# Kernel optimization log

Measured on AMD Instinct MI355X. Metric: run time of the kernel, lower is better.

Reference implementation:

```python
import jax, jax.numpy as jnp
import numpy as np

NUM_CLASSES = 80
NUM_TOP_QUERIES = 300


def setup_inputs() -> dict:
    key = jax.random.key(0)
    k1, k2, k3 = jax.random.split(key, 3)
    N, Q, K = 256, 1000, NUM_CLASSES
    logits = jax.random.normal(k1, (N, Q, K), dtype=jnp.float32)
    boxes = jax.random.uniform(k2, (N, Q, 4), dtype=jnp.float32)  # cxcywh in [0,1]
    original_sizes = jax.random.randint(k3, (N, 2), 1, 1280, dtype=jnp.int32)  # (h, w)
    return {"logits": logits, "boxes": boxes, "original_sizes": original_sizes}


def reference(logits, boxes, original_sizes):
    # cxcywh -> xywh (top-left x,y plus w,h)
    cxcy, wh = boxes[..., :2], boxes[..., 2:]
    boxes_xy = jnp.concatenate([cxcy - wh * 0.5, wh], axis=-1)  # (N, Q, 4)
    # torch code uses only original_sizes[0], flipped (h,w)->(w,h), tiled to (w,h,w,h)
    sizes_wh = jnp.tile(original_sizes[0][::-1].astype(boxes.dtype), 2)  # (4,)
    boxes_xy = boxes_xy * sizes_wh
    # sigmoid scores, flatten class dim into query dim, top-k over Q*K
    N = logits.shape[0]
    scores_flat = jax.nn.sigmoid(logits).reshape(N, -1)  # (N, Q*K)
    scores, index = jax.lax.top_k(scores_flat, NUM_TOP_QUERIES)  # (N, 300)
    labels = index % NUM_CLASSES
    qidx = index // NUM_CLASSES
    # gather selected boxes per batch row
    sel_boxes = jax.vmap(lambda b, i: b[i])(boxes_xy, qidx)  # (N, 300, 4)
    out = jnp.concatenate(
        [labels[..., None].astype(scores.dtype), scores[..., None], sel_boxes], axis=-1
    )  # (N, 300, 6): (class_id, confidence, x, y, w, h)
    return out
```

## Files before the change

kernel.cpp:

```cpp
#include <hip/hip_runtime.h>
#include <stdint.h>


#define TOPK 300
#define NCLS 80
#define NQ 1000
#define QK (NQ * NCLS)
#define NB 2048
#define CAP 2048
#define THREADS 1024
#define LAST_VALID 544
#define T0F 2.4f
#define RNB 512
#define RSH 14

typedef unsigned long long u64;

__device__ __forceinline__ uint32_t ordf(float f) {
  uint32_t u = __float_as_uint(f);
  return (u & 0x80000000u) ? ~u : (u | 0x80000000u);
}
__device__ __forceinline__ float unordf(uint32_t o) {
  uint32_t u = (o & 0x80000000u) ? (o & 0x7fffffffu) : ~o;
  return __uint_as_float(u);
}

__device__ __forceinline__ void rank_emit(
    const u64 key, const uint32_t bin, const uint32_t* rcur,
    const uint32_t* rh, const u64* buf2, const float* boxes, float* out,
    const int n, const float s0, const float s1) {
  const uint32_t end = rcur[bin];
  const uint32_t beg = end - rh[bin];
  uint32_t rank = beg;
  for (uint32_t q = beg; q < end; ++q) rank += (uint32_t)(buf2[q] > key);
  if (rank < TOPK) {
    const uint32_t u = (uint32_t)(key >> 32);
    const uint32_t idx = ~(uint32_t)(key & 0xffffffffu);
    const float lgv = unordf(u);
    const float score = 1.0f / (1.0f + expf(-lgv));
    const uint32_t q = idx / NCLS;
    const uint32_t lab = idx - q * NCLS;
    const float4 b4 = *(const float4*)(boxes + ((size_t)n * NQ + q) * 4);
    float* op = out + ((size_t)n * TOPK + rank) * 6;
    float2* op2 = (float2*)op;
    op2[0] = make_float2((float)lab, score);
    op2[1] = make_float2((b4.x - 0.5f * b4.z) * s1, (b4.y - 0.5f * b4.w) * s0);
    op2[2] = make_float2(b4.z * s1, b4.w * s0);
  }
}

__global__ __launch_bounds__(THREADS) void detr_post_kernel(
    const float* __restrict__ logits, const float* __restrict__ boxes,
    const int* __restrict__ osz, float* __restrict__ out) {
  __shared__ u64 buf[CAP];
  __shared__ u64 smem64[4096];
  __shared__ uint32_t histf[NB];
  __shared__ uint32_t sh_sel[3];
  __shared__ uint32_t sh_cnt;

  uint32_t* const hist4 = (uint32_t*)smem64;
  u64* const buf2 = smem64;
  uint32_t* const rh = (uint32_t*)(smem64 + 2048);
  uint32_t* const rcur = (uint32_t*)(smem64 + 2304);

  const int n = blockIdx.x;
  const int t = threadIdx.x;
  const float* lg = logits + (size_t)n * QK;

  if (t == 0) sh_cnt = 0;
  if (t < RNB) rh[t] = 0;
  __syncthreads();

#pragma unroll 5
  for (int j = 0; j < 19; ++j) {
    const int i = 4 * t + 4096 * j;
    const float4 v = *(const float4*)(lg + i);
    if (v.x >= T0F) {
      const uint32_t p = atomicAdd(&sh_cnt, 1u);
      if (p < CAP) buf[p] = ((u64)ordf(v.x) << 32) | (u64)(~(uint32_t)(i + 0));
    }
    if (v.y >= T0F) {
      const uint32_t p = atomicAdd(&sh_cnt, 1u);
      if (p < CAP) buf[p] = ((u64)ordf(v.y) << 32) | (u64)(~(uint32_t)(i + 1));
    }
    if (v.z >= T0F) {
      const uint32_t p = atomicAdd(&sh_cnt, 1u);
      if (p < CAP) buf[p] = ((u64)ordf(v.z) << 32) | (u64)(~(uint32_t)(i + 2));
    }
    if (v.w >= T0F) {
      const uint32_t p = atomicAdd(&sh_cnt, 1u);
      if (p < CAP) buf[p] = ((u64)ordf(v.w) << 32) | (u64)(~(uint32_t)(i + 3));
    }
  }
  if (t < LAST_VALID) {
    const int i = 4 * t + 4096 * 19;
    const float4 v = *(const float4*)(lg + i);
    if (v.x >= T0F) {
      const uint32_t p = atomicAdd(&sh_cnt, 1u);
      if (p < CAP) buf[p] = ((u64)ordf(v.x) << 32) | (u64)(~(uint32_t)(i + 0));
    }
    if (v.y >= T0F) {
      const uint32_t p = atomicAdd(&sh_cnt, 1u);
      if (p < CAP) buf[p] = ((u64)ordf(v.y) << 32) | (u64)(~(uint32_t)(i + 1));
    }
    if (v.z >= T0F) {
      const uint32_t p = atomicAdd(&sh_cnt, 1u);
      if (p < CAP) buf[p] = ((u64)ordf(v.z) << 32) | (u64)(~(uint32_t)(i + 2));
    }
    if (v.w >= T0F) {
      const uint32_t p = atomicAdd(&sh_cnt, 1u);
      if (p < CAP) buf[p] = ((u64)ordf(v.w) << 32) | (u64)(~(uint32_t)(i + 3));
    }
  }
  __syncthreads();

  uint32_t cnt = sh_cnt;
  const bool fast_ok = (cnt >= TOPK && cnt <= CAP);
  uint32_t baseord = ordf(T0F);

  if (!fast_ok) {
    uint32_t T = 0, S_above = 0, Krem = TOPK;
    int prev_shift = 32;
    const uint32_t sub = (uint32_t)(t & 3);
    const int shifts[3] = {21, 10, 0};
    const int nbns[3] = {2048, 2048, 1024};

    for (int lvl = 0; lvl < 3; ++lvl) {
      const int sh = shifts[lvl];
      const uint32_t nb = (uint32_t)nbns[lvl];

      for (int b = t; b < NB * 4; b += THREADS) hist4[b] = 0;
      __syncthreads();
      for (int j = 0; j < 20; ++j) {
        if (j == 19 && t >= LAST_VALID) break;
        const int i = 4 * t + 4096 * j;
        const float4 v = *(const float4*)(lg + i);
        const float vs[4] = {v.x, v.y, v.z, v.w};
        for (int c = 0; c < 4; ++c) {
          const uint32_t u = ordf(vs[c]);
          if (lvl == 0 || (u >> prev_shift) == (T >> prev_shift))
            atomicAdd(&hist4[(((u >> sh) & (nb - 1)) << 2) | sub], 1u);
        }
      }
      __syncthreads();

      for (uint32_t b = t; b < nb; b += (uint32_t)THREADS) {
        const uint32_t i4 = b << 2;
        histf[b] = hist4[i4] + hist4[i4 + 1] + hist4[i4 + 2] + hist4[i4 + 3];
      }
      __syncthreads();

      for (uint32_t off = 1; off < nb; off <<= 1) {
        uint32_t a0 = histf[t] + ((t + off < nb) ? histf[t + off] : 0u);
        uint32_t a1 = 0;
        if (nb > (uint32_t)THREADS) {
          const uint32_t i1 = (uint32_t)t + THREADS;
          a1 = histf[i1] + ((i1 + off < nb) ? histf[i1 + off] : 0u);
        }
        __syncthreads();
        histf[t] = a0;
        if (nb > (uint32_t)THREADS) histf[(uint32_t)t + THREADS] = a1;
        __syncthreads();
      }

      for (uint32_t b = t; b < nb; b += (uint32_t)THREADS) {
        const uint32_t s = histf[b];
        const uint32_t sn = (b + 1 < nb) ? histf[b + 1] : 0u;
        if (s >= Krem && sn < Krem) {
          sh_sel[0] = b;
          sh_sel[1] = sn;
          sh_sel[2] = s;
        }
      }
      __syncthreads();
      const uint32_t bsel = sh_sel[0], above = sh_sel[1], candL = sh_sel[2];
      __syncthreads();

      T |= bsel << sh;
      if (S_above + candL <= CAP || lvl == 2) break;
      S_above += above;
      Krem -= above;
      prev_shift = sh;
    }

    if (t == 0) sh_cnt = 0;
    __syncthreads();
    if (t < RNB) rh[t] = 0;
    for (int j = 0; j < 20; ++j) {
      if (j == 19 && t >= LAST_VALID) break;
      const int i = 4 * t + 4096 * j;
      const float4 v = *(const float4*)(lg + i);
      const float vs[4] = {v.x, v.y, v.z, v.w};
      for (int c = 0; c < 4; ++c) {
        const uint32_t u = ordf(vs[c]);
        if (u >= T) {
          const uint32_t p = atomicAdd(&sh_cnt, 1u);
          if (p < CAP) buf[p] = ((u64)u << 32) | (u64)(~(uint32_t)(i + c));
        }
      }
    }
    __syncthreads();
    cnt = sh_cnt < CAP ? sh_cnt : CAP;
    baseord = T;
  }

  const u64 k0 = ((uint32_t)t < cnt) ? buf[t] : 0ULL;
  const u64 k1 = ((uint32_t)(t + THREADS) < cnt) ? buf[t + THREADS] : 0ULL;
  uint32_t b0 = 0, b1 = 0;
  if ((uint32_t)t < cnt) {
    b0 = ((uint32_t)(k0 >> 32) - baseord) >> RSH;
    if (b0 > RNB - 1u) b0 = RNB - 1u;
    atomicAdd(&rh[b0], 1u);
  }
  if ((uint32_t)(t + THREADS) < cnt) {
    b1 = ((uint32_t)(k1 >> 32) - baseord) >> RSH;
    if (b1 > RNB - 1u) b1 = RNB - 1u;
    atomicAdd(&rh[b1], 1u);
  }
  __syncthreads();

  if (t < 64) {
    const uint4 a = *(const uint4*)&rh[8 * t];
    const uint4 b = *(const uint4*)&rh[8 * t + 4];
    const uint32_t c0 = a.x, c1 = a.y, c2 = a.z, c3 = a.w;
    const uint32_t c4 = b.x, c5 = b.y, c6 = b.z, c7 = b.w;
    const uint32_t mysum = c0 + c1 + c2 + c3 + c4 + c5 + c6 + c7;
    uint32_t s = mysum;
    for (int d = 1; d < 64; d <<= 1) {
      const uint32_t o = __shfl_down(s, d);
      if (t + d < 64) s += o;
    }
    uint32_t acc = s - mysum;
    rcur[8 * t + 7] = acc; acc += c7;
    rcur[8 * t + 6] = acc; acc += c6;
    rcur[8 * t + 5] = acc; acc += c5;
    rcur[8 * t + 4] = acc; acc += c4;
    rcur[8 * t + 3] = acc; acc += c3;
    rcur[8 * t + 2] = acc; acc += c2;
    rcur[8 * t + 1] = acc; acc += c1;
    rcur[8 * t + 0] = acc;
  }
  __syncthreads();

  if ((uint32_t)t < cnt) {
    const uint32_t s = atomicAdd(&rcur[b0], 1u);
    buf2[s] = k0;
  }
  if ((uint32_t)(t + THREADS) < cnt) {
    const uint32_t s = atomicAdd(&rcur[b1], 1u);
    buf2[s] = k1;
  }
  __syncthreads();

  const float s0 = (float)osz[0];
  const float s1 = (float)osz[1];

  if ((uint32_t)t < cnt)
    rank_emit(k0, b0, rcur, rh, buf2, boxes, out, n, s0, s1);
  if ((uint32_t)(t + THREADS) < cnt)
    rank_emit(k1, b1, rcur, rh, buf2, boxes, out, n, s0, s1);
}

extern "C" void kernel_launch(void* const* d_in, const int* in_sizes, int n_in,
                              void* d_out, int out_size, void* d_ws, size_t ws_size,
                              hipStream_t stream) {
  const float* logits = (const float*)d_in[0];
  const float* boxes = (const float*)d_in[1];
  const int* osz = (const int*)d_in[2];
  float* out = (float*)d_out;
  const int nbatch = in_sizes[0] / QK;
  detr_post_kernel<<<nbatch, THREADS, 0, stream>>>(logits, boxes, osz, out);
}
```

Before: 124.4 us.

## Split threshold scan into multi-block kernel writing candidates to workspace

```diff
diff --git a/kernel.cpp b/kernel.cpp
--- a/kernel.cpp
+++ b/kernel.cpp
@@ -14,6 +14,11 @@
 #define RNB 512
 #define RSH 14
 
+#define SBLK 8
+#define STHREADS 256
+#define SCHUNK 10000
+#define SLAST 196
+
 typedef unsigned long long u64;
 
 __device__ __forceinline__ uint32_t ordf(float f) {
@@ -23,6 +28,51 @@
 __device__ __forceinline__ float unordf(uint32_t o) {
   uint32_t u = (o & 0x80000000u) ? (o & 0x7fffffffu) : ~o;
   return __uint_as_float(u);
+}
+__device__ __forceinline__ u64 mkkey(uint32_t ord, uint32_t idx) {
+  return ((u64)ord << 32) | (u64)(~idx);
+}
+
+__global__ __launch_bounds__(STHREADS) void zero_kernel(
+    uint32_t* __restrict__ cnts, int nbatch) {
+  const int i = blockIdx.x * STHREADS + threadIdx.x;
+  if (i < nbatch) cnts[i] = 0;
+}
+
+__global__ __launch_bounds__(STHREADS) void scan_kernel(
+    const float* __restrict__ logits, u64* __restrict__ cand,
+    uint32_t* __restrict__ cnts) {
+  const int n = blockIdx.x >> 3;
+  const int rb = blockIdx.x & 7;
+  const int t = threadIdx.x;
+  const int coff = rb * SCHUNK;
+  const float* lg = logits + (size_t)n * QK + coff;
+  u64* cnd = cand + (size_t)n * CAP;
+  uint32_t* cp = cnts + n;
+
+#pragma unroll
+  for (int j = 0; j < 10; ++j) {
+    if (j == 9 && t >= SLAST) break;
+    const int i = 4 * (t + STHREADS * j);
+    const float4 v = *(const float4*)(lg + i);
+    const int gi = coff + i;
+    if (v.x >= T0F) {
+      const uint32_t p = atomicAdd(cp, 1u);
+      if (p < CAP) cnd[p] = mkkey(ordf(v.x), (uint32_t)(gi + 0));
+    }
+    if (v.y >= T0F) {
+      const uint32_t p = atomicAdd(cp, 1u);
+      if (p < CAP) cnd[p] = mkkey(ordf(v.y), (uint32_t)(gi + 1));
+    }
+    if (v.z >= T0F) {
+      const uint32_t p = atomicAdd(cp, 1u);
+      if (p < CAP) cnd[p] = mkkey(ordf(v.z), (uint32_t)(gi + 2));
+    }
+    if (v.w >= T0F) {
+      const uint32_t p = atomicAdd(cp, 1u);
+      if (p < CAP) cnd[p] = mkkey(ordf(v.w), (uint32_t)(gi + 3));
+    }
+  }
 }
 
 __device__ __forceinline__ void rank_emit(
@@ -49,9 +99,10 @@
   }
 }
 
-__global__ __launch_bounds__(THREADS) void detr_post_kernel(
+__global__ __launch_bounds__(THREADS) void rank_kernel(
     const float* __restrict__ logits, const float* __restrict__ boxes,
-    const int* __restrict__ osz, float* __restrict__ out) {
+    const int* __restrict__ osz, float* __restrict__ out,
+    const u64* __restrict__ cand, const uint32_t* __restrict__ cnts) {
   __shared__ u64 buf[CAP];
   __shared__ u64 smem64[4096];
   __shared__ uint32_t histf[NB];
@@ -67,58 +118,20 @@
   const int t = threadIdx.x;
   const float* lg = logits + (size_t)n * QK;
 
-  if (t == 0) sh_cnt = 0;
   if (t < RNB) rh[t] = 0;
-  __syncthreads();
-
-#pragma unroll 5
-  for (int j = 0; j < 19; ++j) {
-    const int i = 4 * t + 4096 * j;
-    const float4 v = *(const float4*)(lg + i);
-    if (v.x >= T0F) {
-      const uint32_t p = atomicAdd(&sh_cnt, 1u);
-      if (p < CAP) buf[p] = ((u64)ordf(v.x) << 32) | (u64)(~(uint32_t)(i + 0));
-    }
-    if (v.y >= T0F) {
-      const uint32_t p = atomicAdd(&sh_cnt, 1u);
-      if (p < CAP) buf[p] = ((u64)ordf(v.y) << 32) | (u64)(~(uint32_t)(i + 1));
-    }
-    if (v.z >= T0F) {
-      const uint32_t p = atomicAdd(&sh_cnt, 1u);
-      if (p < CAP) buf[p] = ((u64)ordf(v.z) << 32) | (u64)(~(uint32_t)(i + 2));
-    }
-    if (v.w >= T0F) {
-      const uint32_t p = atomicAdd(&sh_cnt, 1u);
-      if (p < CAP) buf[p] = ((u64)ordf(v.w) << 32) | (u64)(~(uint32_t)(i + 3));
-    }
-  }
-  if (t < LAST_VALID) {
-    const int i = 4 * t + 4096 * 19;
-    const float4 v = *(const float4*)(lg + i);
-    if (v.x >= T0F) {
-      const uint32_t p = atomicAdd(&sh_cnt, 1u);
-      if (p < CAP) buf[p] = ((u64)ordf(v.x) << 32) | (u64)(~(uint32_t)(i + 0));
-    }
-    if (v.y >= T0F) {
-      const uint32_t p = atomicAdd(&sh_cnt, 1u);
-      if (p < CAP) buf[p] = ((u64)ordf(v.y) << 32) | (u64)(~(uint32_t)(i + 1));
-    }
-    if (v.z >= T0F) {
-      const uint32_t p = atomicAdd(&sh_cnt, 1u);
-      if (p < CAP) buf[p] = ((u64)ordf(v.z) << 32) | (u64)(~(uint32_t)(i + 2));
-    }
-    if (v.w >= T0F) {
-      const uint32_t p = atomicAdd(&sh_cnt, 1u);
-      if (p < CAP) buf[p] = ((u64)ordf(v.w) << 32) | (u64)(~(uint32_t)(i + 3));
-    }
-  }
-  __syncthreads();
-
-  uint32_t cnt = sh_cnt;
+
+  uint32_t cnt = cnts[n];
   const bool fast_ok = (cnt >= TOPK && cnt <= CAP);
   uint32_t baseord = ordf(T0F);
 
-  if (!fast_ok) {
+  u64 k0 = 0, k1 = 0;
+  if (fast_ok) {
+    const u64* cnd = cand + (size_t)n * CAP;
+    if ((uint32_t)t < cnt) k0 = cnd[t];
+    if ((uint32_t)(t + THREADS) < cnt) k1 = cnd[t + THREADS];
+    __syncthreads();
+  } else {
+    __syncthreads();
     uint32_t T = 0, S_above = 0, Krem = TOPK;
     int prev_shift = 32;
     const uint32_t sub = (uint32_t)(t & 3);
@@ -195,17 +208,17 @@
         const uint32_t u = ordf(vs[c]);
         if (u >= T) {
           const uint32_t p = atomicAdd(&sh_cnt, 1u);
-          if (p < CAP) buf[p] = ((u64)u << 32) | (u64)(~(uint32_t)(i + c));
+          if (p < CAP) buf[p] = mkkey(u, (uint32_t)(i + c));
         }
       }
     }
     __syncthreads();
     cnt = sh_cnt < CAP ? sh_cnt : CAP;
     baseord = T;
-  }
-
-  const u64 k0 = ((uint32_t)t < cnt) ? buf[t] : 0ULL;
-  const u64 k1 = ((uint32_t)(t + THREADS) < cnt) ? buf[t + THREADS] : 0ULL;
+    if ((uint32_t)t < cnt) k0 = buf[t];
+    if ((uint32_t)(t + THREADS) < cnt) k1 = buf[t + THREADS];
+  }
+
   uint32_t b0 = 0, b1 = 0;
   if ((uint32_t)t < cnt) {
     b0 = ((uint32_t)(k0 >> 32) - baseord) >> RSH;
@@ -261,6 +274,218 @@
     rank_emit(k1, b1, rcur, rh, buf2, boxes, out, n, s0, s1);
 }
 
+__global__ __launch_bounds__(THREADS) void detr_post_mono(
+    const float* __restrict__ logits, const float* __restrict__ boxes,
+    const int* __restrict__ osz, float* __restrict__ out) {
+  __shared__ u64 buf[CAP];
+  __shared__ u64 smem64[4096];
+  __shared__ uint32_t histf[NB];
+  __shared__ uint32_t sh_sel[3];
+  __shared__ uint32_t sh_cnt;
+
+  uint32_t* const hist4 = (uint32_t*)smem64;
+  u64* const buf2 = smem64;
+  uint32_t* const rh = (uint32_t*)(smem64 + 2048);
+  uint32_t* const rcur = (uint32_t*)(smem64 + 2304);
+
+  const int n = blockIdx.x;
+  const int t = threadIdx.x;
+  const float* lg = logits + (size_t)n * QK;
+
+  if (t == 0) sh_cnt = 0;
+  if (t < RNB) rh[t] = 0;
+  __syncthreads();
+
+#pragma unroll 5
+  for (int j = 0; j < 19; ++j) {
+    const int i = 4 * t + 4096 * j;
+    const float4 v = *(const float4*)(lg + i);
+    if (v.x >= T0F) {
+      const uint32_t p = atomicAdd(&sh_cnt, 1u);
+      if (p < CAP) buf[p] = mkkey(ordf(v.x), (uint32_t)(i + 0));
+    }
+    if (v.y >= T0F) {
+      const uint32_t p = atomicAdd(&sh_cnt, 1u);
+      if (p < CAP) buf[p] = mkkey(ordf(v.y), (uint32_t)(i + 1));
+    }
+    if (v.z >= T0F) {
+      const uint32_t p = atomicAdd(&sh_cnt, 1u);
+      if (p < CAP) buf[p] = mkkey(ordf(v.z), (uint32_t)(i + 2));
+    }
+    if (v.w >= T0F) {
+      const uint32_t p = atomicAdd(&sh_cnt, 1u);
+      if (p < CAP) buf[p] = mkkey(ordf(v.w), (uint32_t)(i + 3));
+    }
+  }
+  if (t < LAST_VALID) {
+    const int i = 4 * t + 4096 * 19;
+    const float4 v = *(const float4*)(lg + i);
+    if (v.x >= T0F) {
+      const uint32_t p = atomicAdd(&sh_cnt, 1u);
+      if (p < CAP) buf[p] = mkkey(ordf(v.x), (uint32_t)(i + 0));
+    }
+    if (v.y >= T0F) {
+      const uint32_t p = atomicAdd(&sh_cnt, 1u);
+      if (p < CAP) buf[p] = mkkey(ordf(v.y), (uint32_t)(i + 1));
+    }
+    if (v.z >= T0F) {
+      const uint32_t p = atomicAdd(&sh_cnt, 1u);
+      if (p < CAP) buf[p] = mkkey(ordf(v.z), (uint32_t)(i + 2));
+    }
+    if (v.w >= T0F) {
+      const uint32_t p = atomicAdd(&sh_cnt, 1u);
+      if (p < CAP) buf[p] = mkkey(ordf(v.w), (uint32_t)(i + 3));
+    }
+  }
+  __syncthreads();
+
+  uint32_t cnt = sh_cnt;
+  const bool fast_ok = (cnt >= TOPK && cnt <= CAP);
+  uint32_t baseord = ordf(T0F);
+
+  if (!fast_ok) {
+    uint32_t T = 0, S_above = 0, Krem = TOPK;
+    int prev_shift = 32;
+    const uint32_t sub = (uint32_t)(t & 3);
+    const int shifts[3] = {21, 10, 0};
+    const int nbns[3] = {2048, 2048, 1024};
+
+    for (int lvl = 0; lvl < 3; ++lvl) {
+      const int sh = shifts[lvl];
+      const uint32_t nb = (uint32_t)nbns[lvl];
+
+      for (int b = t; b < NB * 4; b += THREADS) hist4[b] = 0;
+      __syncthreads();
+      for (int j = 0; j < 20; ++j) {
+        if (j == 19 && t >= LAST_VALID) break;
+        const int i = 4 * t + 4096 * j;
+        const float4 v = *(const float4*)(lg + i);
+        const float vs[4] = {v.x, v.y, v.z, v.w};
+        for (int c = 0; c < 4; ++c) {
+          const uint32_t u = ordf(vs[c]);
+          if (lvl == 0 || (u >> prev_shift) == (T >> prev_shift))
+            atomicAdd(&hist4[(((u >> sh) & (nb - 1)) << 2) | sub], 1u);
+        }
+      }
+      __syncthreads();
+
+      for (uint32_t b = t; b < nb; b += (uint32_t)THREADS) {
+        const uint32_t i4 = b << 2;
+        histf[b] = hist4[i4] + hist4[i4 + 1] + hist4[i4 + 2] + hist4[i4 + 3];
+      }
+      __syncthreads();
+
+      for (uint32_t off = 1; off < nb; off <<= 1) {
+        uint32_t a0 = histf[t] + ((t + off < nb) ? histf[t + off] : 0u);
+        uint32_t a1 = 0;
+        if (nb > (uint32_t)THREADS) {
+          const uint32_t i1 = (uint32_t)t + THREADS;
+          a1 = histf[i1] + ((i1 + off < nb) ? histf[i1 + off] : 0u);
+        }
+        __syncthreads();
+        histf[t] = a0;
+        if (nb > (uint32_t)THREADS) histf[(uint32_t)t + THREADS] = a1;
+        __syncthreads();
+      }
+
+      for (uint32_t b = t; b < nb; b += (uint32_t)THREADS) {
+        const uint32_t s = histf[b];
+        const uint32_t sn = (b + 1 < nb) ? histf[b + 1] : 0u;
+        if (s >= Krem && sn < Krem) {
+          sh_sel[0] = b;
+          sh_sel[1] = sn;
+          sh_sel[2] = s;
+        }
+      }
+      __syncthreads();
+      const uint32_t bsel = sh_sel[0], above = sh_sel[1], candL = sh_sel[2];
+      __syncthreads();
+
+      T |= bsel << sh;
+      if (S_above + candL <= CAP || lvl == 2) break;
+      S_above += above;
+      Krem -= above;
+      prev_shift = sh;
+    }
+
+    if (t == 0) sh_cnt = 0;
+    __syncthreads();
+    if (t < RNB) rh[t] = 0;
+    for (int j = 0; j < 20; ++j) {
+      if (j == 19 && t >= LAST_VALID) break;
+      const int i = 4 * t + 4096 * j;
+      const float4 v = *(const float4*)(lg + i);
+      const float vs[4] = {v.x, v.y, v.z, v.w};
+      for (int c = 0; c < 4; ++c) {
+        const uint32_t u = ordf(vs[c]);
+        if (u >= T) {
+          const uint32_t p = atomicAdd(&sh_cnt, 1u);
+          if (p < CAP) buf[p] = mkkey(u, (uint32_t)(i + c));
+        }
+      }
+    }
+    __syncthreads();
+    cnt = sh_cnt < CAP ? sh_cnt : CAP;
+    baseord = T;
+  }
+
+  const u64 k0 = ((uint32_t)t < cnt) ? buf[t] : 0ULL;
+  const u64 k1 = ((uint32_t)(t + THREADS) < cnt) ? buf[t + THREADS] : 0ULL;
+  uint32_t b0 = 0, b1 = 0;
+  if ((uint32_t)t < cnt) {
+    b0 = ((uint32_t)(k0 >> 32) - baseord) >> RSH;
+    if (b0 > RNB - 1u) b0 = RNB - 1u;
+    atomicAdd(&rh[b0], 1u);
+  }
+  if ((uint32_t)(t + THREADS) < cnt) {
+    b1 = ((uint32_t)(k1 >> 32) - baseord) >> RSH;
+    if (b1 > RNB - 1u) b1 = RNB - 1u;
+    atomicAdd(&rh[b1], 1u);
+  }
+  __syncthreads();
+
+  if (t < 64) {
+    const uint4 a = *(const uint4*)&rh[8 * t];
+    const uint4 b = *(const uint4*)&rh[8 * t + 4];
+    const uint32_t c0 = a.x, c1 = a.y, c2 = a.z, c3 = a.w;
+    const uint32_t c4 = b.x, c5 = b.y, c6 = b.z, c7 = b.w;
+    const uint32_t mysum = c0 + c1 + c2 + c3 + c4 + c5 + c6 + c7;
+    uint32_t s = mysum;
+    for (int d = 1; d < 64; d <<= 1) {
+      const uint32_t o = __shfl_down(s, d);
+      if (t + d < 64) s += o;
+    }
+    uint32_t acc = s - mysum;
+    rcur[8 * t + 7] = acc; acc += c7;
+    rcur[8 * t + 6] = acc; acc += c6;
+    rcur[8 * t + 5] = acc; acc += c5;
+    rcur[8 * t + 4] = acc; acc += c4;
+    rcur[8 * t + 3] = acc; acc += c3;
+    rcur[8 * t + 2] = acc; acc += c2;
+    rcur[8 * t + 1] = acc; acc += c1;
+    rcur[8 * t + 0] = acc;
+  }
+  __syncthreads();
+
+  if ((uint32_t)t < cnt) {
+    const uint32_t s = atomicAdd(&rcur[b0], 1u);
+    buf2[s] = k0;
+  }
+  if ((uint32_t)(t + THREADS) < cnt) {
+    const uint32_t s = atomicAdd(&rcur[b1], 1u);
+    buf2[s] = k1;
+  }
+  __syncthreads();
+
+  const float s0 = (float)osz[0];
+  const float s1 = (float)osz[1];
+
+  if ((uint32_t)t < cnt)
+    rank_emit(k0, b0, rcur, rh, buf2, boxes, out, n, s0, s1);
+  if ((uint32_t)(t + THREADS) < cnt)
+    rank_emit(k1, b1, rcur, rh, buf2, boxes, out, n, s0, s1);
+}
+
 extern "C" void kernel_launch(void* const* d_in, const int* in_sizes, int n_in,
                               void* d_out, int out_size, void* d_ws, size_t ws_size,
                               hipStream_t stream) {
@@ -269,5 +494,18 @@
   const int* osz = (const int*)d_in[2];
   float* out = (float*)d_out;
   const int nbatch = in_sizes[0] / QK;
-  detr_post_kernel<<<nbatch, THREADS, 0, stream>>>(logits, boxes, osz, out);
-}
+
+  const size_t cnt_bytes = 1024;
+  const size_t need = cnt_bytes + (size_t)nbatch * CAP * sizeof(u64);
+  if (d_ws != nullptr && ws_size >= need && (size_t)nbatch * 4 <= cnt_bytes) {
+    uint32_t* cnts = (uint32_t*)d_ws;
+    u64* cand = (u64*)((char*)d_ws + cnt_bytes);
+    const int zblocks = (nbatch + STHREADS - 1) / STHREADS;
+    zero_kernel<<<zblocks, STHREADS, 0, stream>>>(cnts, nbatch);
+    scan_kernel<<<nbatch * SBLK, STHREADS, 0, stream>>>(logits, cand, cnts);
+    rank_kernel<<<nbatch, THREADS, 0, stream>>>(logits, boxes, osz, out, cand,
+                                                cnts);
+  } else {
+    detr_post_mono<<<nbatch, THREADS, 0, stream>>>(logits, boxes, osz, out);
+  }
+}
```

Measured after the change: 263.9 us. 112% more time.
